# Performance work log

Measured on AMD Instinct MI355X. Metric: run time of the kernel, lower is better.

Reference implementation:

```python
import jax, jax.numpy as jnp
import numpy as np
from jax import lax

DIM = 768
HEADS = 12
EXPERTS = 4
CAPS = [0.4, 0.3, 0.2, 0.1]  # capacity fraction per expert e=0..E-1 (e=E-1 is the full-dim expert)
EPS = 1e-5


def _layernorm(x, g, b):
    mu = jnp.mean(x, axis=-1, keepdims=True)
    var = jnp.mean(jnp.square(x - mu), axis=-1, keepdims=True)
    return (x - mu) * lax.rsqrt(var + EPS) * g + b


def _route(x, router_w, router_b):
    # Expert-preferred capacity router: experts (largest dim first) greedily take
    # their top-capacity tokens by router probability among still-unassigned tokens.
    B, N, _ = x.shape
    probs = jax.nn.softmax(x @ router_w + router_b, axis=-1)  # [B,N,E]
    ks = [int(c * N) for c in CAPS]
    ks[-1] += N - sum(ks)  # remainder to the largest expert
    assigned = jnp.zeros((B, N), dtype=jnp.int32)
    avail = jnp.ones((B, N), dtype=bool)
    brow = jnp.arange(B)[:, None]
    for e in reversed(range(EXPERTS)):
        pe = jnp.where(avail, probs[:, :, e], -jnp.inf)
        _, idx = lax.top_k(pe, ks[e])  # [B, k_e]
        sel = jnp.zeros((B, N), dtype=bool).at[brow, idx].set(True)
        assigned = jnp.where(sel, e, assigned)
        avail = avail & ~sel
    router_probs = jnp.take_along_axis(probs, assigned[..., None], axis=-1)[..., 0]  # [B,N]
    return assigned, router_probs


def _feat_mask(token_mask, dtype):
    # expert e uses the first DIM / 2^(E-1-e) features (nested slicing)
    dims = jnp.array([DIM >> (EXPERTS - 1 - e) for e in range(EXPERTS)], dtype=jnp.int32)
    d_tok = dims[token_mask]  # [B,N]
    return (jnp.arange(DIM)[None, None, :] < d_tok[..., None]).astype(dtype)  # [B,N,D]


def _nested_attention(h, mask, wqkv, bqkv, wo, bo):
    # masking input + output of a full projection == using the top-left nested submatrix
    B, N, D = h.shape
    hd = D // HEADS
    qkv = ((h * mask) @ wqkv + bqkv) * jnp.tile(mask, (1, 1, 3))  # [B,N,3D]
    q, k, v = jnp.split(qkv, 3, axis=-1)
    q = q.reshape(B, N, HEADS, hd).transpose(0, 2, 1, 3)  # [B,H,N,hd]
    k = k.reshape(B, N, HEADS, hd).transpose(0, 2, 1, 3)
    v = v.reshape(B, N, HEADS, hd).transpose(0, 2, 1, 3)
    scores = jnp.einsum('bhqd,bhkd->bhqk', q, k) * (hd ** -0.5)
    attn = jax.nn.softmax(scores, axis=-1)
    out = jnp.einsum('bhqk,bhkd->bhqd', attn, v)  # [B,H,N,hd]
    out = out.transpose(0, 2, 1, 3).reshape(B, N, D) * mask
    return ((out @ wo) + bo) * mask


def setup_inputs() -> dict:
    key = jax.random.key(0)
    ks = jax.random.split(key, 8)
    B, N, D = 4, 1024, DIM
    s = 0.02
    return {
        'x': jax.random.normal(ks[0], (B, N, D), jnp.float32),
        'ln1_g': jnp.ones((D,), jnp.float32),
        'ln1_b': jnp.zeros((D,), jnp.float32),
        'router_w': jax.random.normal(ks[1], (D, EXPERTS), jnp.float32) * s,
        'router_b': jnp.zeros((EXPERTS,), jnp.float32),
        'wqkv': jax.random.normal(ks[2], (D, 3 * D), jnp.float32) * s,
        'bqkv': jnp.zeros((3 * D,), jnp.float32),
        'wo': jax.random.normal(ks[3], (D, D), jnp.float32) * s,
        'bo': jnp.zeros((D,), jnp.float32),
        'ln2_g': jnp.ones((D,), jnp.float32),
        'ln2_b': jnp.zeros((D,), jnp.float32),
        'w1': jax.random.normal(ks[4], (D, 4 * D), jnp.float32) * s,
        'b1': jnp.zeros((4 * D,), jnp.float32),
        'w2': jax.random.normal(ks[5], (4 * D, D), jnp.float32) * s,
        'b2': jnp.zeros((D,), jnp.float32),
    }


def reference(x, ln1_g, ln1_b, router_w, router_b, wqkv, bqkv, wo, bo,
              ln2_g, ln2_b, w1, b1, w2, b2):
    token_mask, router_probs = _route(x, router_w, router_b)
    mask = _feat_mask(token_mask, x.dtype)  # [B,N,D]
    z = x + _nested_attention(_layernorm(x, ln1_g, ln1_b), mask, wqkv, bqkv, wo, bo)
    h2 = _layernorm(z, ln2_g, ln2_b)
    z_prime = jax.nn.gelu(h2 @ w1 + b1, approximate=False) @ w2 + b2
    # probability-weighted token combine
    return z + router_probs[..., None] * z_prime
```

## Files before the change

### kernel.cpp

```cpp
#include <hip/hip_runtime.h>
#include <math.h>

#define DIM 768
#define NTOK 1024
#define BATCH 4
#define HEADS 12
#define TOKENS (BATCH * NTOK)

typedef __bf16 bf16;
typedef __attribute__((ext_vector_type(8))) __bf16 bf16x8;
typedef __attribute__((ext_vector_type(4))) float floatx4;

__device__ __forceinline__ void async_ld16(const bf16* g, bf16* l) {
    __builtin_amdgcn_global_load_lds((const __attribute__((address_space(1))) unsigned int*)g,
                                     (__attribute__((address_space(3))) unsigned int*)l, 16, 0, 0);
}

__global__ __launch_bounds__(256) void prep_kernel(const float* __restrict__ wqkv,
                                                   const float* __restrict__ wo,
                                                   const float* __restrict__ w1,
                                                   const float* __restrict__ w2,
                                                   bf16* __restrict__ o0, bf16* __restrict__ o1,
                                                   bf16* __restrict__ o2, bf16* __restrict__ o3,
                                                   const float* __restrict__ x,
                                                   const float* __restrict__ rw,
                                                   const float* __restrict__ rb,
                                                   float* __restrict__ probs) {
    int id = blockIdx.x;
    if (id >= 6912) {
        int t = (id - 6912) * 4 + (threadIdx.x >> 6);
        int lane = threadIdx.x & 63;
        const float* xr = x + (size_t)t * DIM;
        double acc[4] = {0, 0, 0, 0};
#pragma unroll
        for (int i = 0; i < 12; ++i) {
            int k = lane + i * 64;
            double xv = (double)xr[k];
            floatx4 w = *(const floatx4*)&rw[k * 4];
            acc[0] += xv * (double)w[0];
            acc[1] += xv * (double)w[1];
            acc[2] += xv * (double)w[2];
            acc[3] += xv * (double)w[3];
        }
#pragma unroll
        for (int m = 1; m < 64; m <<= 1) {
#pragma unroll
            for (int e = 0; e < 4; ++e) acc[e] += __shfl_xor(acc[e], m);
        }
        if (lane == 0) {
            double lg[4];
            for (int e = 0; e < 4; ++e) lg[e] = acc[e] + (double)rb[e];
            double mx = lg[0];
            for (int e = 1; e < 4; ++e) mx = fmax(mx, lg[e]);
            double s = 0.0, p[4];
            for (int e = 0; e < 4; ++e) { p[e] = exp(lg[e] - mx); s += p[e]; }
            for (int e = 0; e < 4; ++e) probs[(size_t)t * 4 + e] = (float)(p[e] / s);
        }
        return;
    }
    const float* W;
    bf16* Wt;
    int K, N, bx, by;
    if (id < 1728) { W = wqkv; Wt = o0; K = 768; N = 2304; bx = id % 72; by = id / 72; }
    else if (id < 2304) { int r = id - 1728; W = wo; Wt = o1; K = 768; N = 768; bx = r % 24; by = r / 24; }
    else if (id < 4608) { int r = id - 2304; W = w1; Wt = o2; K = 768; N = 3072; bx = r % 96; by = r / 96; }
    else { int r = id - 4608; W = w2; Wt = o3; K = 3072; N = 768; bx = r % 24; by = r / 24; }
    __shared__ float t[32][33];
    int x0 = bx * 32, y0 = by * 32;
    int tx = threadIdx.x & 31, ty = threadIdx.x >> 5;
#pragma unroll
    for (int i = 0; i < 4; ++i)
        t[ty + i * 8][tx] = W[(size_t)(y0 + ty + i * 8) * N + x0 + tx];
    __syncthreads();
#pragma unroll
    for (int i = 0; i < 4; ++i)
        Wt[(size_t)(x0 + ty + i * 8) * K + y0 + tx] = (bf16)t[tx][ty + i * 8];
}

template <int E, int KCAP, bool FIRST, bool LAST>
__global__ __launch_bounds__(256) void route_pass(const float* __restrict__ probs,
                                                  int* __restrict__ avail,
                                                  int* __restrict__ dtok_g,
                                                  float* __restrict__ rprobs_g) {
    int b = blockIdx.y;
    int i = blockIdx.x * 256 + threadIdx.x;
    const float* pb = probs + (size_t)b * NTOK * 4;
    __shared__ float sp[1024];
    for (int j = threadIdx.x; j < 1024; j += 256) {
        bool av = FIRST ? true : (avail[b * NTOK + j] != 0);
        sp[j] = av ? pb[j * 4 + E] : -INFINITY;
    }
    __syncthreads();
    bool av_i = FIRST ? true : (avail[b * NTOK + i] != 0);
    float pi = sp[i];
    int cnt = 0;
#pragma unroll 8
    for (int j0 = 0; j0 < 1024; j0 += 4) {
        floatx4 pj = *(const floatx4*)&sp[j0];
        cnt += (pj[0] > pi) || (pj[0] == pi && (j0 + 0) < i);
        cnt += (pj[1] > pi) || (pj[1] == pi && (j0 + 1) < i);
        cnt += (pj[2] > pi) || (pj[2] == pi && (j0 + 2) < i);
        cnt += (pj[3] > pi) || (pj[3] == pi && (j0 + 3) < i);
    }
    bool sel = av_i && (cnt < KCAP);
    if (sel) {
        dtok_g[b * NTOK + i] = DIM >> (3 - E);
        rprobs_g[b * NTOK + i] = pb[i * 4 + E];
    } else if (LAST && av_i) {
        dtok_g[b * NTOK + i] = DIM >> 3;
        rprobs_g[b * NTOK + i] = pb[i * 4 + 0];
    }
    if (!LAST) {
        if (FIRST) avail[b * NTOK + i] = sel ? 0 : 1;
        else if (sel) avail[b * NTOK + i] = 0;
    }
}

__global__ __launch_bounds__(256) void ln_mask_kernel(const float* __restrict__ x,
                                                      const float* __restrict__ g,
                                                      const float* __restrict__ bta,
                                                      const int* __restrict__ dtok,
                                                      bf16* __restrict__ out) {
    int t = blockIdx.x;
    int tid = threadIdx.x;
    int lane = tid & 63, wv = tid >> 6;
    const float* xr = x + (size_t)t * DIM;
    float v0 = xr[tid], v1 = xr[tid + 256], v2 = xr[tid + 512];
    float s = v0 + v1 + v2;
#pragma unroll
    for (int m = 1; m < 64; m <<= 1) s += __shfl_xor(s, m);
    __shared__ float ws1[4], ws2[4];
    if (lane == 0) ws1[wv] = s;
    __syncthreads();
    float mu = (ws1[0] + ws1[1] + ws1[2] + ws1[3]) * (1.0f / DIM);
    float d0 = v0 - mu, d1 = v1 - mu, d2 = v2 - mu;
    float v = d0 * d0 + d1 * d1 + d2 * d2;
#pragma unroll
    for (int m = 1; m < 64; m <<= 1) v += __shfl_xor(v, m);
    if (lane == 0) ws2[wv] = v;
    __syncthreads();
    float rs = rsqrtf((ws2[0] + ws2[1] + ws2[2] + ws2[3]) * (1.0f / DIM) + 1e-5f);
    int d = dtok ? dtok[t] : DIM;
    out[(size_t)t * DIM + tid] = (bf16)((tid < d) ? d0 * rs * g[tid] + bta[tid] : 0.0f);
    out[(size_t)t * DIM + tid + 256] =
        (bf16)((tid + 256 < d) ? d1 * rs * g[tid + 256] + bta[tid + 256] : 0.0f);
    out[(size_t)t * DIM + tid + 512] =
        (bf16)((tid + 512 < d) ? d2 * rs * g[tid + 512] + bta[tid + 512] : 0.0f);
}

template <int MODE>
__global__ __launch_bounds__(256) void gemm_mfma(const bf16* __restrict__ A,
                                                 const bf16* __restrict__ Bt,
                                                 const float* __restrict__ bias,
                                                 void* __restrict__ Cout,
                                                 int M, int NN, int K,
                                                 const int* __restrict__ dtok,
                                                 const float* __restrict__ aux,
                                                 const float* __restrict__ rp,
                                                 bf16* __restrict__ vtg) {
    __shared__ bf16 As[2][64 * 32];
    __shared__ bf16 Bs[2][128 * 32];
    int m0 = blockIdx.x * 64;
    int n0 = blockIdx.y * 128;
    int tid = threadIdx.x;
    int wv = tid >> 6;
    int lane = tid & 63;
    int l16 = lane & 15, q4 = lane >> 4;
    int wm = (wv >> 1) * 32, wn = (wv & 1) * 64;
    int srow = lane >> 2;
    int scol = (((lane & 3) ^ (srow & 3)) * 8);
    const bf16* gA0 = A + (size_t)(m0 + 16 * wv + srow) * K + scol;
    const bf16* gB0 = Bt + (size_t)(n0 + 32 * wv + srow) * K + scol;
    const bf16* gB1 = gB0 + (size_t)16 * K;
    int a0 = (16 * wv) * 32;
    int b0 = (32 * wv) * 32, b1 = (32 * wv + 16) * 32;
    async_ld16(gA0, &As[0][a0]);
    async_ld16(gB0, &Bs[0][b0]);
    async_ld16(gB1, &Bs[0][b1]);
    gA0 += 32; gB0 += 32; gB1 += 32;
    __syncthreads();
    floatx4 acc[2][4] = {};
    int kIters = K / 32;
    int cur = 0;
    bool vb = (MODE == 0) && (n0 >= 1536);
    for (int it = 0; it < kIters; ++it) {
        if (it + 1 < kIters) {
            async_ld16(gA0, &As[cur ^ 1][a0]);
            async_ld16(gB0, &Bs[cur ^ 1][b0]);
            async_ld16(gB1, &Bs[cur ^ 1][b1]);
            gA0 += 32; gB0 += 32; gB1 += 32;
        }
        int gsl = (q4 ^ (l16 & 3)) * 8;
        bf16x8 af[2], bfr[4];
#pragma unroll
        for (int t = 0; t < 2; ++t)
            af[t] = *(const bf16x8*)&As[cur][(wm + t * 16 + l16) * 32 + gsl];
#pragma unroll
        for (int t = 0; t < 4; ++t)
            bfr[t] = *(const bf16x8*)&Bs[cur][(wn + t * 16 + l16) * 32 + gsl];
        if (vb) {
#pragma unroll
            for (int i = 0; i < 2; ++i)
#pragma unroll
                for (int j = 0; j < 4; ++j)
                    acc[i][j] =
                        __builtin_amdgcn_mfma_f32_16x16x32_bf16(bfr[j], af[i], acc[i][j], 0, 0, 0);
        } else {
#pragma unroll
            for (int i = 0; i < 2; ++i)
#pragma unroll
                for (int j = 0; j < 4; ++j)
                    acc[i][j] =
                        __builtin_amdgcn_mfma_f32_16x16x32_bf16(af[i], bfr[j], acc[i][j], 0, 0, 0);
        }
        __syncthreads();
        cur ^= 1;
    }
    if (MODE == 0 && n0 >= 1536) {
#pragma unroll
        for (int i = 0; i < 2; ++i) {
            int tok = m0 + wm + i * 16 + l16;
            int dt_tok = dtok[tok];
            int b = tok >> 10, n = tok & 1023;
#pragma unroll
            for (int j = 0; j < 4; ++j) {
#pragma unroll
                for (int r = 0; r < 4; ++r) {
                    int col = n0 + wn + j * 16 + q4 * 4 + r;
                    int vcol = col - 1536;
                    float c = acc[i][j][r] + bias[col];
                    c = (vcol < dt_tok) ? c : 0.0f;
                    int h = vcol >> 6, d = vcol & 63;
                    vtg[(size_t)((b * HEADS + h) * 64 + d) * NTOK + n] = (bf16)c;
                }
            }
        }
        return;
    }
#pragma unroll
    for (int i = 0; i < 2; ++i) {
#pragma unroll
        for (int j = 0; j < 4; ++j) {
            int col = n0 + wn + j * 16 + l16;
#pragma unroll
            for (int r = 0; r < 4; ++r) {
                int row = m0 + wm + i * 16 + q4 * 4 + r;
                if (MODE == 0) {
                    float c = acc[i][j][r] + bias[col];
                    int jm = col % 768;
                    c = (jm < dtok[row]) ? c : 0.0f;
                    ((bf16*)Cout)[(size_t)row * NN + col] = (bf16)c;
                } else if (MODE == 1) {
                    float c = acc[i][j][r] + bias[col];
                    c = (col < dtok[row]) ? c : 0.0f;
                    c += aux[(size_t)row * DIM + col];
                    ((float*)Cout)[(size_t)row * NN + col] = c;
                } else if (MODE == 2) {
                    float c = acc[i][j][r] + bias[col];
                    c = 0.5f * c * (1.0f + erff(c * 0.70710678118654752f));
                    ((bf16*)Cout)[(size_t)row * NN + col] = (bf16)c;
                } else {
                    float c = acc[i][j][r] + bias[col];
                    ((float*)Cout)[(size_t)row * NN + col] =
                        aux[(size_t)row * DIM + col] + rp[row] * c;
                }
            }
        }
    }
}

#define LDH 72
__global__ __launch_bounds__(256) void attn_mfma(const bf16* __restrict__ qkv,
                                                 const bf16* __restrict__ vtg,
                                                 const int* __restrict__ dtok,
                                                 bf16* __restrict__ attno) {
    int qt = blockIdx.x;
    int h = blockIdx.y;
    int b = blockIdx.z;
    int tid = threadIdx.x;
    int wv = tid >> 6;
    int lane = tid & 63;
    int l16 = lane & 15, q4 = lane >> 4;
    __shared__ bf16 Qs[64 * LDH];
    __shared__ bf16 Ks[64 * LDH];
    __shared__ bf16 Vt[64 * LDH];
    __shared__ bf16 Ps[4][16 * LDH];
    size_t base = (size_t)b * NTOK * 2304;
    size_t vbase = ((size_t)(b * HEADS + h)) * 64 * NTOK;
#pragma unroll
    for (int u = 0; u < 2; ++u) {
        int row = (u * 256 + tid) >> 3, part = (u * 256 + tid) & 7;
        *(floatx4*)&Qs[row * LDH + part * 8] =
            *(const floatx4*)&qkv[base + (size_t)(qt * 64 + row) * 2304 + h * 64 + part * 8];
    }
    floatx4 o[4] = {};
    float psum[4] = {0.0f, 0.0f, 0.0f, 0.0f};
    floatx4 kreg[2], vreg[2];
#pragma unroll
    for (int u = 0; u < 2; ++u) {
        int row = (u * 256 + tid) >> 3, part = (u * 256 + tid) & 7;
        kreg[u] = *(const floatx4*)&qkv[base + (size_t)row * 2304 + 768 + h * 64 + part * 8];
        vreg[u] = *(const floatx4*)&vtg[vbase + (size_t)row * NTOK + part * 8];
    }
    for (int kt = 0; kt < 16; ++kt) {
        __syncthreads();
#pragma unroll
        for (int u = 0; u < 2; ++u) {
            int row = (u * 256 + tid) >> 3, part = (u * 256 + tid) & 7;
            *(floatx4*)&Ks[row * LDH + part * 8] = kreg[u];
            *(floatx4*)&Vt[row * LDH + part * 8] = vreg[u];
        }
        __syncthreads();
        if (kt < 15) {
#pragma unroll
            for (int u = 0; u < 2; ++u) {
                int row = (u * 256 + tid) >> 3, part = (u * 256 + tid) & 7;
                kreg[u] = *(const floatx4*)&qkv[base + (size_t)((kt + 1) * 64 + row) * 2304 + 768 +
                                                h * 64 + part * 8];
                vreg[u] = *(const floatx4*)&vtg[vbase + (size_t)row * NTOK + (kt + 1) * 64 + part * 8];
            }
        }
        floatx4 sc[4] = {};
#pragma unroll
        for (int ch = 0; ch < 2; ++ch) {
            bf16x8 aq = *(const bf16x8*)&Qs[(wv * 16 + l16) * LDH + ch * 32 + q4 * 8];
#pragma unroll
            for (int nt = 0; nt < 4; ++nt) {
                bf16x8 bk = *(const bf16x8*)&Ks[(nt * 16 + l16) * LDH + ch * 32 + q4 * 8];
                sc[nt] = __builtin_amdgcn_mfma_f32_16x16x32_bf16(aq, bk, sc[nt], 0, 0, 0);
            }
        }
#pragma unroll
        for (int nt = 0; nt < 4; ++nt)
#pragma unroll
            for (int r = 0; r < 4; ++r) {
                float p = __expf(sc[nt][r] * 0.125f);
                psum[r] += p;
                Ps[wv][(q4 * 4 + r) * LDH + nt * 16 + l16] = (bf16)p;
            }
#pragma unroll
        for (int ch = 0; ch < 2; ++ch) {
            bf16x8 ap = *(const bf16x8*)&Ps[wv][l16 * LDH + ch * 32 + q4 * 8];
#pragma unroll
            for (int dt = 0; dt < 4; ++dt) {
                bf16x8 bv = *(const bf16x8*)&Vt[(dt * 16 + l16) * LDH + ch * 32 + q4 * 8];
                o[dt] = __builtin_amdgcn_mfma_f32_16x16x32_bf16(ap, bv, o[dt], 0, 0, 0);
            }
        }
    }
#pragma unroll
    for (int r = 0; r < 4; ++r) {
        float s = psum[r];
#pragma unroll
        for (int msk = 1; msk < 16; msk <<= 1) s += __shfl_xor(s, msk);
        int tokrow = qt * 64 + wv * 16 + q4 * 4 + r;
        int dt_tok = dtok[b * NTOK + tokrow];
        float inv = 1.0f / s;
#pragma unroll
        for (int dt = 0; dt < 4; ++dt) {
            int col = h * 64 + dt * 16 + l16;
            float val = (col < dt_tok) ? o[dt][r] * inv : 0.0f;
            attno[((size_t)b * NTOK + tokrow) * DIM + col] = (bf16)val;
        }
    }
}

extern "C" void kernel_launch(void* const* d_in, const int* in_sizes, int n_in,
                              void* d_out, int out_size, void* d_ws, size_t ws_size,
                              hipStream_t stream) {
    const float* x = (const float*)d_in[0];
    const float* ln1g = (const float*)d_in[1];
    const float* ln1b = (const float*)d_in[2];
    const float* rw = (const float*)d_in[3];
    const float* rb = (const float*)d_in[4];
    const float* wqkv = (const float*)d_in[5];
    const float* bqkv = (const float*)d_in[6];
    const float* wo = (const float*)d_in[7];
    const float* bo = (const float*)d_in[8];
    const float* ln2g = (const float*)d_in[9];
    const float* ln2b = (const float*)d_in[10];
    const float* w1 = (const float*)d_in[11];
    const float* b1 = (const float*)d_in[12];
    const float* w2 = (const float*)d_in[13];
    const float* b2 = (const float*)d_in[14];
    float* out = (float*)d_out;

    char* ws = (char*)d_ws;
    size_t off = 0;
    auto alloc = [&](size_t bytes) {
        void* p = ws + off;
        off = (off + bytes + 255) & ~(size_t)255;
        return p;
    };
    bf16* h1m = (bf16*)alloc(sizeof(bf16) * TOKENS * DIM);
    float* probs = (float*)alloc(sizeof(float) * TOKENS * 4);
    float* rprobs = (float*)alloc(sizeof(float) * TOKENS);
    int* dtok = (int*)alloc(sizeof(int) * TOKENS);
    int* avail = (int*)alloc(sizeof(int) * TOKENS);
    bf16* qkvb = (bf16*)alloc(sizeof(bf16) * TOKENS * 3 * DIM);
    bf16* vtg = (bf16*)alloc(sizeof(bf16) * BATCH * HEADS * 64 * NTOK);
    bf16* attno = (bf16*)alloc(sizeof(bf16) * TOKENS * DIM);
    float* z = (float*)alloc(sizeof(float) * TOKENS * DIM);
    bf16* h2 = (bf16*)alloc(sizeof(bf16) * TOKENS * DIM);
    bf16* ffn1 = (bf16*)alloc(sizeof(bf16) * TOKENS * 4 * DIM);
    bf16* wqkvT = (bf16*)alloc(sizeof(bf16) * DIM * 3 * DIM);
    bf16* woT = (bf16*)alloc(sizeof(bf16) * DIM * DIM);
    bf16* w1T = (bf16*)alloc(sizeof(bf16) * DIM * 4 * DIM);
    bf16* w2T = (bf16*)alloc(sizeof(bf16) * 4 * DIM * DIM);

    prep_kernel<<<6912 + TOKENS / 4, 256, 0, stream>>>(wqkv, wo, w1, w2, wqkvT, woT, w1T, w2T,
                                                       x, rw, rb, probs);
    route_pass<3, 104, true, false><<<dim3(4, BATCH), 256, 0, stream>>>(probs, avail, dtok, rprobs);
    route_pass<2, 204, false, false><<<dim3(4, BATCH), 256, 0, stream>>>(probs, avail, dtok, rprobs);
    route_pass<1, 307, false, true><<<dim3(4, BATCH), 256, 0, stream>>>(probs, avail, dtok, rprobs);
    ln_mask_kernel<<<TOKENS, 256, 0, stream>>>(x, ln1g, ln1b, dtok, h1m);
    gemm_mfma<0><<<dim3(4096 / 64, 2304 / 128), 256, 0, stream>>>(
        h1m, wqkvT, bqkv, qkvb, TOKENS, 2304, 768, dtok, nullptr, nullptr, vtg);
    attn_mfma<<<dim3(16, HEADS, BATCH), 256, 0, stream>>>(qkvb, vtg, dtok, attno);
    gemm_mfma<1><<<dim3(4096 / 64, 768 / 128), 256, 0, stream>>>(
        attno, woT, bo, z, TOKENS, 768, 768, dtok, x, nullptr, nullptr);
    ln_mask_kernel<<<TOKENS, 256, 0, stream>>>(z, ln2g, ln2b, nullptr, h2);
    gemm_mfma<2><<<dim3(4096 / 64, 3072 / 128), 256, 0, stream>>>(
        h2, w1T, b1, ffn1, TOKENS, 3072, 768, nullptr, nullptr, nullptr, nullptr);
    gemm_mfma<3><<<dim3(4096 / 64, 768 / 128), 256, 0, stream>>>(
        ffn1, w2T, b2, out, TOKENS, 768, 3072, nullptr, z, rprobs, nullptr);
}
```

Baseline: 406.5 us.

## Triple-buffer GEMM LDS tiles with a single barrier and explicit vmcnt waits

Moves the MFMA GEMM from a double-buffered to a triple-buffered LDS pipeline. Two tiles are prefetched ahead, and each iteration uses one s_barrier guarded by an explicit s_waitcnt vmcnt instead of two __syncthreads. The XOR swizzle on the LDS layout is also dropped, so rows are stored and read with plain column offsets. This should hide more global-load latency and remove a barrier per K step, but it uses 50% more LDS and the unswizzled reads may bring back LDS bank conflicts.

```diff
diff --git a/kernel.cpp b/kernel.cpp
--- a/kernel.cpp
+++ b/kernel.cpp
@@ -158,8 +158,8 @@
                                                  const float* __restrict__ aux,
                                                  const float* __restrict__ rp,
                                                  bf16* __restrict__ vtg) {
-    __shared__ bf16 As[2][64 * 32];
-    __shared__ bf16 Bs[2][128 * 32];
+    __shared__ bf16 As[3][64 * 32];
+    __shared__ bf16 Bs[3][128 * 32];
     int m0 = blockIdx.x * 64;
     int n0 = blockIdx.y * 128;
     int tid = threadIdx.x;
@@ -167,37 +167,44 @@
     int lane = tid & 63;
     int l16 = lane & 15, q4 = lane >> 4;
     int wm = (wv >> 1) * 32, wn = (wv & 1) * 64;
-    int srow = lane >> 2;
-    int scol = (((lane & 3) ^ (srow & 3)) * 8);
-    const bf16* gA0 = A + (size_t)(m0 + 16 * wv + srow) * K + scol;
+    int srow = lane >> 2, scol = (lane & 3) * 8;
+    const bf16* gA = A + (size_t)(m0 + 16 * wv + srow) * K + scol;
     const bf16* gB0 = Bt + (size_t)(n0 + 32 * wv + srow) * K + scol;
     const bf16* gB1 = gB0 + (size_t)16 * K;
     int a0 = (16 * wv) * 32;
     int b0 = (32 * wv) * 32, b1 = (32 * wv + 16) * 32;
-    async_ld16(gA0, &As[0][a0]);
+    int kIters = K / 32;
+    async_ld16(gA, &As[0][a0]);
     async_ld16(gB0, &Bs[0][b0]);
     async_ld16(gB1, &Bs[0][b1]);
-    gA0 += 32; gB0 += 32; gB1 += 32;
-    __syncthreads();
+    gA += 32; gB0 += 32; gB1 += 32;
+    async_ld16(gA, &As[1][a0]);
+    async_ld16(gB0, &Bs[1][b0]);
+    async_ld16(gB1, &Bs[1][b1]);
+    gA += 32; gB0 += 32; gB1 += 32;
     floatx4 acc[2][4] = {};
-    int kIters = K / 32;
-    int cur = 0;
+    int cur = 0, nxt2 = 2;
     bool vb = (MODE == 0) && (n0 >= 1536);
     for (int it = 0; it < kIters; ++it) {
         if (it + 1 < kIters) {
-            async_ld16(gA0, &As[cur ^ 1][a0]);
-            async_ld16(gB0, &Bs[cur ^ 1][b0]);
-            async_ld16(gB1, &Bs[cur ^ 1][b1]);
-            gA0 += 32; gB0 += 32; gB1 += 32;
-        }
-        int gsl = (q4 ^ (l16 & 3)) * 8;
+            asm volatile("s_waitcnt vmcnt(3)" ::: "memory");
+        } else {
+            asm volatile("s_waitcnt vmcnt(0)" ::: "memory");
+        }
+        asm volatile("s_barrier" ::: "memory");
+        if (it + 2 < kIters) {
+            async_ld16(gA, &As[nxt2][a0]);
+            async_ld16(gB0, &Bs[nxt2][b0]);
+            async_ld16(gB1, &Bs[nxt2][b1]);
+            gA += 32; gB0 += 32; gB1 += 32;
+        }
         bf16x8 af[2], bfr[4];
 #pragma unroll
         for (int t = 0; t < 2; ++t)
-            af[t] = *(const bf16x8*)&As[cur][(wm + t * 16 + l16) * 32 + gsl];
+            af[t] = *(const bf16x8*)&As[cur][(wm + t * 16 + l16) * 32 + q4 * 8];
 #pragma unroll
         for (int t = 0; t < 4; ++t)
-            bfr[t] = *(const bf16x8*)&Bs[cur][(wn + t * 16 + l16) * 32 + gsl];
+            bfr[t] = *(const bf16x8*)&Bs[cur][(wn + t * 16 + l16) * 32 + q4 * 8];
         if (vb) {
 #pragma unroll
             for (int i = 0; i < 2; ++i)
@@ -213,8 +220,8 @@
                     acc[i][j] =
                         __builtin_amdgcn_mfma_f32_16x16x32_bf16(af[i], bfr[j], acc[i][j], 0, 0, 0);
         }
-        __syncthreads();
-        cur ^= 1;
+        cur = (cur == 2) ? 0 : cur + 1;
+        nxt2 = (nxt2 == 2) ? 0 : nxt2 + 1;
     }
     if (MODE == 0 && n0 >= 1536) {
 #pragma unroll
```

Result: no change. 411.2 us (+1.2%).
